# Performance work log

Hardware: AMD Instinct MI355X
Metric: run time of the kernel (lower is better)

The kernel has to match this reference:

```python
import jax, jax.numpy as jnp
import numpy as np

N_NODES = 100000
N_EDGES = 800000
NUM_GRAPHS = 512
IN_DIM = 16
EDGE_DIM = 1
HID = 64       # emb_dim
MLP_H = 32     # hidden_layers inside each MPNNLayer
L = 3          # num_layers
EPS = 1e-5


def setup_inputs() -> dict:
    key = jax.random.key(0)
    ks = jax.random.split(key, 24)
    s = 0.05
    inp = {
        "x": jax.random.normal(ks[0], (N_NODES, IN_DIM), jnp.float32),
        "edge_index": jax.random.randint(ks[1], (2, N_EDGES), 0, N_NODES),
        "edge_attr": jax.random.uniform(ks[2], (N_EDGES, EDGE_DIM), jnp.float32),
        "batch": jnp.sort(jax.random.randint(ks[3], (N_NODES,), 0, NUM_GRAPHS)),
        # input projection
        "lin_in_w": jax.random.normal(ks[4], (IN_DIM, HID), jnp.float32) * s,
        "lin_in_b": jnp.zeros((HID,), jnp.float32),
        # message MLP (stacked over L layers): Linear(129->32), BN(32), ReLU, Linear(32->64), ReLU, BN(64)
        "msg_w1": jax.random.normal(ks[5], (L, 2 * HID + EDGE_DIM, MLP_H), jnp.float32) * s,
        "msg_b1": jnp.zeros((L, MLP_H), jnp.float32),
        "msg_g1": jnp.ones((L, MLP_H), jnp.float32),
        "msg_be1": jnp.zeros((L, MLP_H), jnp.float32),
        "msg_w2": jax.random.normal(ks[6], (L, MLP_H, HID), jnp.float32) * s,
        "msg_b2": jnp.zeros((L, HID), jnp.float32),
        "msg_g2": jnp.ones((L, HID), jnp.float32),
        "msg_be2": jnp.zeros((L, HID), jnp.float32),
        # update MLP: Linear(128->32), BN(32), ReLU, Linear(32->64), ReLU, BN(64)
        "upd_w1": jax.random.normal(ks[7], (L, 2 * HID, MLP_H), jnp.float32) * s,
        "upd_b1": jnp.zeros((L, MLP_H), jnp.float32),
        "upd_g1": jnp.ones((L, MLP_H), jnp.float32),
        "upd_be1": jnp.zeros((L, MLP_H), jnp.float32),
        "upd_w2": jax.random.normal(ks[8], (L, MLP_H, HID), jnp.float32) * s,
        "upd_b2": jnp.zeros((L, HID), jnp.float32),
        "upd_g2": jnp.ones((L, HID), jnp.float32),
        "upd_be2": jnp.zeros((L, HID), jnp.float32),
        # head Linear(64->1) + ReLU
        "out_w": jax.random.normal(ks[9], (HID, 1), jnp.float32) * s,
        "out_b": jnp.zeros((1,), jnp.float32),
    }
    return inp


def _bn(h, g, b):
    # BatchNorm1d, training-mode batch stats (biased variance), dropout treated as identity (eval)
    mu = jnp.mean(h, axis=0)
    var = jnp.var(h, axis=0)
    return g * (h - mu) * jax.lax.rsqrt(var + EPS) + b


def reference(x, edge_index, edge_attr, batch,
              lin_in_w, lin_in_b,
              msg_w1, msg_b1, msg_g1, msg_be1, msg_w2, msg_b2, msg_g2, msg_be2,
              upd_w1, upd_b1, upd_g1, upd_be1, upd_w2, upd_b2, upd_g2, upd_be2,
              out_w, out_b):
    src = edge_index[0]  # x_j source
    dst = edge_index[1]  # x_i target / aggregation index
    h = x @ lin_in_w + lin_in_b  # [N, HID]
    for l in range(L):
        # message: cat([x_i, x_j, edge_attr]) -> Linear -> BN -> ReLU -> Linear -> ReLU -> BN
        m_in = jnp.concatenate([h[dst], h[src], edge_attr], axis=1)  # [E, 2*HID+EDGE_DIM]
        m = jax.nn.relu(_bn(m_in @ msg_w1[l] + msg_b1[l], msg_g1[l], msg_be1[l]))
        m = _bn(jax.nn.relu(m @ msg_w2[l] + msg_b2[l]), msg_g2[l], msg_be2[l])
        # aggregate: scatter-add over destination nodes
        agg = jax.ops.segment_sum(m, dst, num_segments=N_NODES)  # [N, HID]
        # update: cat([x, aggr]) -> Linear -> BN -> ReLU -> Linear -> ReLU -> BN
        u_in = jnp.concatenate([h, agg], axis=1)  # [N, 2*HID]
        u = jax.nn.relu(_bn(u_in @ upd_w1[l] + upd_b1[l], upd_g1[l], upd_be1[l]))
        u = _bn(jax.nn.relu(u @ upd_w2[l] + upd_b2[l]), upd_g2[l], upd_be2[l])
        h = h + u  # residual (x += conv(...))
    # global mean pool
    pooled = jax.ops.segment_sum(h, batch, num_segments=NUM_GRAPHS)
    counts = jax.ops.segment_sum(jnp.ones((h.shape[0],), h.dtype), batch, num_segments=NUM_GRAPHS)
    pooled = pooled / jnp.maximum(counts, 1.0)[:, None]
    return jax.nn.relu(pooled @ out_w + out_b).reshape(-1)  # [NUM_GRAPHS]
```

## Files before the change

### kernel.cpp

```cpp
#include <hip/hip_runtime.h>
#include <hip/hip_bf16.h>

#define N_NODES   100000
#define N_EDGES   800000
#define NUM_GRAPHS 512
#define IN_DIM    16
#define HID       64
#define MLP_H     32
#define EPS       1e-5f
#define TPB       256
#define SCAN_B    1024
#define NCHUNK    ((N_NODES + SCAN_B - 1) / SCAN_B)
#define GSB       2048
#define NWAVES    (GSB * 4)
#define PER_W     ((N_EDGES + NWAVES - 1) / NWAVES)
#define NODEBLKS  ((N_NODES + 63) / 64)

using nh2   = decltype(__builtin_amdgcn_cvt_pkrtz(0.f, 0.f));
typedef _Float16 f16x8 __attribute__((ext_vector_type(8)));
typedef float    f32x4 __attribute__((ext_vector_type(4)));
typedef int      i32x4 __attribute__((ext_vector_type(4)));

__device__ __forceinline__ nh2 pack2(float a, float b) {
  return __builtin_amdgcn_cvt_pkrtz(a, b);
}
__device__ __forceinline__ float wsum(float v) {
  v += __shfl_xor(v, 1, 64);
  v += __shfl_xor(v, 2, 64);
  v += __shfl_xor(v, 4, 64);
  v += __shfl_xor(v, 8, 64);
  v += __shfl_xor(v, 16, 64);
  v += __shfl_xor(v, 32, 64);
  return v;
}
__device__ __forceinline__ int lbound(const int* __restrict__ rs, int key) {
  int lo = 0, hi = N_NODES;
  while (lo < hi) { int m = (lo + hi) >> 1; if (rs[m] < key) lo = m + 1; else hi = m; }
  return lo;
}

__global__ __launch_bounds__(TPB) void k_deg(const int* __restrict__ ei, int* __restrict__ deg) {
  int e = blockIdx.x * TPB + threadIdx.x;
  if (e < N_EDGES) atomicAdd(&deg[ei[N_EDGES + e]], 1);
}

__global__ __launch_bounds__(SCAN_B) void k_scan_part(const int* __restrict__ deg,
                                                      int* __restrict__ partials) {
  __shared__ int red[SCAN_B];
  int i = blockIdx.x * SCAN_B + threadIdx.x;
  red[threadIdx.x] = (i < N_NODES) ? deg[i] : 0;
  __syncthreads();
  for (int off = SCAN_B / 2; off > 0; off >>= 1) {
    if (threadIdx.x < off) red[threadIdx.x] += red[threadIdx.x + off];
    __syncthreads();
  }
  if (threadIdx.x == 0) partials[blockIdx.x] = red[0];
}

__global__ void k_scan_mid(int* __restrict__ partials, int* __restrict__ row_start) {
  int run = 0;
  for (int b = 0; b < NCHUNK; ++b) { int t = partials[b]; partials[b] = run; run += t; }
  row_start[N_NODES] = run;
}

__global__ __launch_bounds__(SCAN_B) void k_scan_fin(const int* __restrict__ deg,
                                                     const int* __restrict__ partials,
                                                     int* __restrict__ row_start,
                                                     int* __restrict__ cursor) {
  __shared__ int buf[2][SCAN_B];
  int t = threadIdx.x, i = blockIdx.x * SCAN_B + t;
  int v = (i < N_NODES) ? deg[i] : 0;
  buf[0][t] = v;
  __syncthreads();
  int cur = 0;
  for (int off = 1; off < SCAN_B; off <<= 1) {
    int nv = buf[cur][t] + ((t >= off) ? buf[cur][t - off] : 0);
    buf[cur ^ 1][t] = nv; cur ^= 1;
    __syncthreads();
  }
  if (i < N_NODES) {
    int excl = buf[cur][t] - v + partials[blockIdx.x];
    row_start[i] = excl;
    cursor[i] = excl;
  }
}

__global__ __launch_bounds__(TPB) void k_fill(const int* __restrict__ ei,
                                              const float* __restrict__ ea,
                                              int* __restrict__ cursor,
                                              i32x4* __restrict__ erec) {
  int e = blockIdx.x * TPB + threadIdx.x;
  if (e >= N_EDGES) return;
  int dst = ei[N_EDGES + e];
  int pos = atomicAdd(&cursor[dst], 1);
  i32x4 rec;
  rec[0] = ei[e];
  rec[1] = dst;
  rec[2] = __float_as_int(ea[e]);
  rec[3] = 0;
  erec[pos] = rec;
}

__global__ __launch_bounds__(TPB) void k_lin_in(const float* __restrict__ x,
                                                const float* __restrict__ w,
                                                const float* __restrict__ b,
                                                float* __restrict__ h) {
  int i = blockIdx.x * TPB + threadIdx.x;
  if (i >= N_NODES) return;
  float xi[IN_DIM];
  const float4* xp = reinterpret_cast<const float4*>(x + i * IN_DIM);
#pragma unroll
  for (int q = 0; q < 4; ++q) {
    float4 v = xp[q];
    xi[4*q] = v.x; xi[4*q+1] = v.y; xi[4*q+2] = v.z; xi[4*q+3] = v.w;
  }
  float4* hp = reinterpret_cast<float4*>(h + i * HID);
#pragma unroll
  for (int j4 = 0; j4 < HID/4; ++j4) {
    float o[4];
#pragma unroll
    for (int c = 0; c < 4; ++c) {
      int j = j4*4 + c;
      float acc = b[j];
#pragma unroll
      for (int k = 0; k < IN_DIM; ++k) acc += xi[k] * w[k*HID + j];
      o[c] = acc;
    }
    float4 ov = {o[0], o[1], o[2], o[3]};
    hp[j4] = ov;
  }
}

__global__ __launch_bounds__(TPB) void k_pq(const float* __restrict__ h,
                                            const float* __restrict__ w1,
                                            const float* __restrict__ b1,
                                            _Float16* __restrict__ Ph,
                                            _Float16* __restrict__ Qh) {
  const int part = __builtin_amdgcn_readfirstlane(threadIdx.x >> 6);
  const int lane = threadIdx.x & 63;
  const int i = blockIdx.x * 64 + lane;
  if (i >= N_NODES) return;
  const int jb = (part & 1) * 16;
  const bool isQ = part >= 2;
  const float* wbase = w1 + (isQ ? 64 * MLP_H : 0) + jb;
  float acc[16];
#pragma unroll
  for (int j = 0; j < 16; ++j) acc[j] = isQ ? 0.f : b1[jb + j];
  const float4* hp = reinterpret_cast<const float4*>(h + i * HID);
#pragma unroll 4
  for (int k4 = 0; k4 < 16; ++k4) {
    float4 a = hp[k4];
    const float* wr = wbase + (k4*4) * MLP_H;
#pragma unroll
    for (int j = 0; j < 16; ++j)
      acc[j] += a.x*wr[j] + a.y*wr[MLP_H+j] + a.z*wr[2*MLP_H+j] + a.w*wr[3*MLP_H+j];
  }
  _Float16* dst = isQ ? Qh : Ph;
  i32x4 o0, o1;
#pragma unroll
  for (int c = 0; c < 4; ++c) {
    o0[c] = __builtin_bit_cast(int, pack2(acc[2*c],   acc[2*c+1]));
    o1[c] = __builtin_bit_cast(int, pack2(acc[8+2*c], acc[8+2*c+1]));
  }
  i32x4* qp = reinterpret_cast<i32x4*>(dst + i * MLP_H + jb);
  qp[0] = o0; qp[1] = o1;
}

__global__ __launch_bounds__(TPB) void k_gather(const _Float16* __restrict__ Ph,
                                                const _Float16* __restrict__ Qh,
                                                const i32x4* __restrict__ erec,
                                                const float* __restrict__ w1,
                                                _Float16* __restrict__ z1h,
                                                float* __restrict__ gstat) {
  const int lane = threadIdx.x & 63;
  const int kq  = lane & 15;
  const int qtr = lane >> 4;
  const float wk0 = w1[128 * MLP_H + 2*kq];
  const float wk1 = w1[128 * MLP_H + 2*kq + 1];
  const int* Qi = (const int*)Qh;
  const int* Pi = (const int*)Ph;
  int* z1i = (int*)z1h;
  float s0 = 0.f, s1 = 0.f, qa0 = 0.f, qa1 = 0.f;
  const int wv = blockIdx.x * 4 + (threadIdx.x >> 6);
  const int c0 = wv * PER_W;
  const int c1 = min(c0 + PER_W, N_EDGES);
  if (c0 < N_EDGES) {
    const int c1m1 = c1 - 1;
    const int rounds = (c1 - c0 + 3) >> 2;
#define EIDX(R) min(c0 + 4*(R) + qtr, c1m1)
    i32x4 rec2 = erec[EIDX(0)];
    i32x4 rec3 = erec[EIDX(1)];
    i32x4 recH = erec[EIDX(2)];
    int   qiA = Qi[rec2[0] * 16 + kq];
    int   piA = Pi[rec2[1] * 16 + kq];
    float aA  = __int_as_float(rec2[2]);
    int   qiB = Qi[rec3[0] * 16 + kq];
    int   piB = Pi[rec3[1] * 16 + kq];
    float aB  = __int_as_float(rec3[2]);
    for (int r = 0; r < rounds; ++r) {
      i32x4 recN = erec[EIDX(r + 3)];
      int   qiC = Qi[recH[0] * 16 + kq];
      int   piC = Pi[recH[1] * 16 + kq];
      float aC  = __int_as_float(recH[2]);
      const int e = c0 + 4*r + qtr;
      nh2 hv = __builtin_bit_cast(nh2, qiA);
      nh2 pv = __builtin_bit_cast(nh2, piA);
      float z0 = (float)pv.x + (float)hv.x + aA * wk0;
      float z1 = (float)pv.y + (float)hv.y + aA * wk1;
      if (e < c1) {
        z1i[min(e, c1m1) * 16 + kq] = __builtin_bit_cast(int, pack2(z0, z1));
        s0 += z0; s1 += z1;
        qa0 = fmaf(z0, z0, qa0); qa1 = fmaf(z1, z1, qa1);
      }
      qiA = qiB; piA = piB; aA = aB;
      qiB = qiC; piB = piC; aB = aC;
      recH = recN;
    }
#undef EIDX
  }
  s0  += __shfl_xor(s0, 16, 64);  s0  += __shfl_xor(s0, 32, 64);
  s1  += __shfl_xor(s1, 16, 64);  s1  += __shfl_xor(s1, 32, 64);
  qa0 += __shfl_xor(qa0, 16, 64); qa0 += __shfl_xor(qa0, 32, 64);
  qa1 += __shfl_xor(qa1, 16, 64); qa1 += __shfl_xor(qa1, 32, 64);
  __shared__ float ls[4][MLP_H], lq[4][MLP_H];
  const int w = threadIdx.x >> 6;
  if (lane < 16) {
    ls[w][2*lane] = s0; ls[w][2*lane+1] = s1;
    lq[w][2*lane] = qa0; lq[w][2*lane+1] = qa1;
  }
  __syncthreads();
  const int t = threadIdx.x;
  if (t < MLP_H)
    unsafeAtomicAdd(&gstat[t], ls[0][t] + ls[1][t] + ls[2][t] + ls[3][t]);
  else if (t < 2*MLP_H)
    unsafeAtomicAdd(&gstat[t], lq[0][t-MLP_H] + lq[1][t-MLP_H] + lq[2][t-MLP_H] + lq[3][t-MLP_H]);
}

__global__ __launch_bounds__(TPB) void k_msgdot(const _Float16* __restrict__ z1h,
                                                const int* __restrict__ rs,
                                                const float* __restrict__ gstat_in,
                                                const float* __restrict__ g1,
                                                const float* __restrict__ be1,
                                                const float* __restrict__ w2,
                                                const float* __restrict__ b2,
                                                float* __restrict__ agg,
                                                float* __restrict__ gstat_out) {
  const int lane = threadIdx.x & 63;
  const int col = lane & 15;
  const int g   = lane >> 4;
  float a1v[8], c1v[8];
#pragma unroll
  for (int i = 0; i < 8; ++i) {
    int kf = g*8 + i;
    float mu = gstat_in[kf] * (1.f / N_EDGES);
    float var = fmaxf(gstat_in[MLP_H + kf] * (1.f / N_EDGES) - mu * mu, 0.f);
    float a = g1[kf] * rsqrtf(var + EPS);
    a1v[i] = a; c1v[i] = be1[kf] - a * mu;
  }
  f16x8 bf0, bf1, bf2, bf3;
#define MKB(BF, C) { i32x4 bw; \
  _Pragma("unroll") for (int ii = 0; ii < 4; ++ii) { \
    nh2 p = pack2(w2[(g*8 + 2*ii) * HID + (C)*16 + col], \
                  w2[(g*8 + 2*ii + 1) * HID + (C)*16 + col]); \
    bw[ii] = __builtin_bit_cast(int, p); } \
  BF = __builtin_bit_cast(f16x8, bw); }
  MKB(bf0, 0) MKB(bf1, 1) MKB(bf2, 2) MKB(bf3, 3)
#undef MKB
  float b2c[4];
#pragma unroll
  for (int c = 0; c < 4; ++c) b2c[c] = b2[c*16 + col];

  float sacc[4] = {0.f,0.f,0.f,0.f}, qacc[4] = {0.f,0.f,0.f,0.f};
  const int wv = blockIdx.x * 4 + (threadIdx.x >> 6);
  const int key0 = min(wv * PER_W, N_EDGES);
  const int key1 = min((wv + 1) * PER_W, N_EDGES);
  const int n0 = lbound(rs, key0);
  const int n1 = (wv == NWAVES - 1) ? N_NODES : lbound(rs, key1);

  if (n0 < n1) {
    const int eLast = rs[n1] - 1;
    f16x8 zv = *reinterpret_cast<const f16x8*>(z1h + min(rs[n0] + col, eLast) * MLP_H + g * 8);
    for (int n = n0; n < n1; ++n) {
      const int start = rs[n], end = rs[n + 1];
      float aggacc[4] = {0.f,0.f,0.f,0.f};
      for (int t0 = start; t0 < end; t0 += 16) {
        const int bnext = (t0 + 16 < end) ? (t0 + 16) : end;
        f16x8 zvN = *reinterpret_cast<const f16x8*>(z1h + min(bnext + col, eLast) * MLP_H + g * 8);
        i32x4 aw;
#pragma unroll
        for (int i = 0; i < 4; ++i) {
          float m0 = fmaxf(fmaf(a1v[2*i],   (float)zv[2*i],   c1v[2*i]),   0.f);
          float m1 = fmaxf(fmaf(a1v[2*i+1], (float)zv[2*i+1], c1v[2*i+1]), 0.f);
          aw[i] = __builtin_bit_cast(int, pack2(m0, m1));
        }
        f16x8 af = __builtin_bit_cast(f16x8, aw);
        f32x4 zc = {0.f,0.f,0.f,0.f};
        f32x4 cc0 = __builtin_amdgcn_mfma_f32_16x16x32_f16(af, bf0, zc, 0, 0, 0);
        f32x4 cc1 = __builtin_amdgcn_mfma_f32_16x16x32_f16(af, bf1, zc, 0, 0, 0);
        f32x4 cc2 = __builtin_amdgcn_mfma_f32_16x16x32_f16(af, bf2, zc, 0, 0, 0);
        f32x4 cc3 = __builtin_amdgcn_mfma_f32_16x16x32_f16(af, bf3, zc, 0, 0, 0);
        bool vld[4];
#pragma unroll
        for (int reg = 0; reg < 4; ++reg) vld[reg] = (t0 + g*4 + reg) < end;
#define EPI(CC, CI) { \
  _Pragma("unroll") for (int reg = 0; reg < 4; ++reg) { \
    float tv = fmaxf(CC[reg] + b2c[CI], 0.f); \
    tv = vld[reg] ? tv : 0.f; \
    aggacc[CI] += tv; qacc[CI] = fmaf(tv, tv, qacc[CI]); } }
        EPI(cc0, 0) EPI(cc1, 1) EPI(cc2, 2) EPI(cc3, 3)
#undef EPI
        zv = zvN;
      }
#pragma unroll
      for (int c = 0; c < 4; ++c) sacc[c] += aggacc[c];
#pragma unroll
      for (int c = 0; c < 4; ++c) {
        aggacc[c] += __shfl_xor(aggacc[c], 16, 64);
        aggacc[c] += __shfl_xor(aggacc[c], 32, 64);
      }
      float aout = (g == 0) ? aggacc[0] : (g == 1) ? aggacc[1] : (g == 2) ? aggacc[2] : aggacc[3];
      agg[n * HID + g * 16 + col] = aout;
    }
  }
#pragma unroll
  for (int c = 0; c < 4; ++c) {
    sacc[c] += __shfl_xor(sacc[c], 16, 64);
    sacc[c] += __shfl_xor(sacc[c], 32, 64);
    qacc[c] += __shfl_xor(qacc[c], 16, 64);
    qacc[c] += __shfl_xor(qacc[c], 32, 64);
  }
  __shared__ float ls[4][HID], lq[4][HID];
  const int w = threadIdx.x >> 6;
  if (g == 0) {
#pragma unroll
    for (int c = 0; c < 4; ++c) { ls[w][c*16 + col] = sacc[c]; lq[w][c*16 + col] = qacc[c]; }
  }
  __syncthreads();
  const int t = threadIdx.x;
  if (t < HID)
    unsafeAtomicAdd(&gstat_out[t], ls[0][t] + ls[1][t] + ls[2][t] + ls[3][t]);
  else if (t < 2*HID)
    unsafeAtomicAdd(&gstat_out[t], lq[0][t-HID] + lq[1][t-HID] + lq[2][t-HID] + lq[3][t-HID]);
}

__global__ __launch_bounds__(TPB) void k_upd1(const float* __restrict__ h,
                                              const float* __restrict__ agg,
                                              const int* __restrict__ deg,
                                              const float* __restrict__ gstat_in,
                                              const float* __restrict__ g2,
                                              const float* __restrict__ be2,
                                              const float* __restrict__ w1,
                                              const float* __restrict__ b1,
                                              float* __restrict__ zu1) {
  __shared__ float sa[HID], sc[HID];
  {
    int t = threadIdx.x;
    if (t < HID) {
      float mu = gstat_in[t] * (1.f / N_EDGES);
      float var = fmaxf(gstat_in[HID + t] * (1.f / N_EDGES) - mu * mu, 0.f);
      float a = g2[t] * rsqrtf(var + EPS);
      sa[t] = a; sc[t] = be2[t] - a * mu;
    }
  }
  __syncthreads();
  const int widx = __builtin_amdgcn_readfirstlane(threadIdx.x >> 6);
  const int part = widx & 1;
  const int grp  = blockIdx.x * 2 + (widx >> 1);
  const int lane = threadIdx.x & 63;
  const int jb = part * 16;
  const int i = grp * 64 + lane;
  if (i >= N_NODES) return;
  float acc[16];
#pragma unroll
  for (int j = 0; j < 16; ++j) acc[j] = b1[jb + j];
  const float4* hp = reinterpret_cast<const float4*>(h + i * HID);
#pragma unroll 4
  for (int k4 = 0; k4 < 16; ++k4) {
    float4 a = hp[k4];
    const float* wr = w1 + (k4*4) * MLP_H + jb;
#pragma unroll
    for (int j = 0; j < 16; ++j)
      acc[j] += a.x*wr[j] + a.y*wr[MLP_H+j] + a.z*wr[2*MLP_H+j] + a.w*wr[3*MLP_H+j];
  }
  float degf = (float)deg[i];
  const float4* ap = reinterpret_cast<const float4*>(agg + i * HID);
#pragma unroll 4
  for (int k4 = 0; k4 < 16; ++k4) {
    float4 g4 = ap[k4];
    int k = k4*4;
    float a0 = sa[k]  *g4.x + sc[k]  *degf;
    float a1 = sa[k+1]*g4.y + sc[k+1]*degf;
    float a2 = sa[k+2]*g4.z + sc[k+2]*degf;
    float a3 = sa[k+3]*g4.w + sc[k+3]*degf;
    const float* wr = w1 + (64 + k) * MLP_H + jb;
#pragma unroll
    for (int j = 0; j < 16; ++j)
      acc[j] += a0*wr[j] + a1*wr[MLP_H+j] + a2*wr[2*MLP_H+j] + a3*wr[3*MLP_H+j];
  }
  float4* zp = reinterpret_cast<float4*>(zu1 + i * MLP_H + jb);
#pragma unroll
  for (int c = 0; c < 4; ++c) {
    float4 o = {acc[4*c], acc[4*c+1], acc[4*c+2], acc[4*c+3]};
    zp[c] = o;
  }
}

__global__ __launch_bounds__(TPB) void k_upd2(const float* __restrict__ zu1,
                                              const float* __restrict__ gstat_in,
                                              const float* __restrict__ gu1,
                                              const float* __restrict__ beu1,
                                              const float* __restrict__ w2,
                                              const float* __restrict__ b2,
                                              float* __restrict__ tu) {
  __shared__ float sa[MLP_H], sc[MLP_H];
  {
    int t = threadIdx.x;
    if (t < MLP_H) {
      float mu = gstat_in[t] * (1.f / N_NODES);
      float var = fmaxf(gstat_in[MLP_H + t] * (1.f / N_NODES) - mu * mu, 0.f);
      float a = gu1[t] * rsqrtf(var + EPS);
      sa[t] = a; sc[t] = beu1[t] - a * mu;
    }
  }
  __syncthreads();
  const int widx = __builtin_amdgcn_readfirstlane(threadIdx.x >> 6);
  const int part = widx & 1;
  const int grp  = blockIdx.x * 2 + (widx >> 1);
  const int lane = threadIdx.x & 63;
  const int jb = part * 32;
  const int i = grp * 64 + lane;
  if (i >= N_NODES) return;
  float m1[MLP_H];
  const float4* zp = reinterpret_cast<const float4*>(zu1 + i * MLP_H);
#pragma unroll
  for (int c = 0; c < MLP_H/4; ++c) {
    float4 z = zp[c];
    int kk = 4*c;
    m1[kk]   = fmaxf(sa[kk]  *z.x + sc[kk],   0.f);
    m1[kk+1] = fmaxf(sa[kk+1]*z.y + sc[kk+1], 0.f);
    m1[kk+2] = fmaxf(sa[kk+2]*z.z + sc[kk+2], 0.f);
    m1[kk+3] = fmaxf(sa[kk+3]*z.w + sc[kk+3], 0.f);
  }
#pragma unroll
  for (int j4 = 0; j4 < 8; ++j4) {
    float tv[4];
#pragma unroll
    for (int c = 0; c < 4; ++c) {
      int j = jb + j4*4 + c;
      float v = b2[j];
#pragma unroll
      for (int kk = 0; kk < MLP_H; ++kk) v += m1[kk] * w2[kk*HID + j];
      tv[c] = fmaxf(v, 0.f);
    }
    float4 o = {tv[0], tv[1], tv[2], tv[3]};
    *reinterpret_cast<float4*>(tu + i * HID + jb + j4*4) = o;
  }
}

template <int NF>
__global__ __launch_bounds__(TPB) void k_colstats(const float* __restrict__ X,
                                                  int nrows, float* __restrict__ gstat) {
  const int RPB = TPB / NF;
  int f = threadIdx.x % NF;
  int rloc = threadIdx.x / NF;
  float s = 0.f, q = 0.f;
  for (int r = blockIdx.x * RPB + rloc; r < nrows; r += gridDim.x * RPB) {
    float v = X[r * NF + f];
    s += v; q = fmaf(v, v, q);
  }
  __shared__ float ls[TPB], lq[TPB];
  ls[threadIdx.x] = s; lq[threadIdx.x] = q;
  __syncthreads();
  if (threadIdx.x < NF) {
    float ss = 0.f, qq = 0.f;
#pragma unroll
    for (int r = 0; r < RPB; ++r) { ss += ls[r*NF + f]; qq += lq[r*NF + f]; }
    unsafeAtomicAdd(&gstat[f], ss);
    unsafeAtomicAdd(&gstat[NF + f], qq);
  }
}

__global__ __launch_bounds__(TPB) void k_resid(float* __restrict__ h,
                                               const float* __restrict__ tu,
                                               const float* __restrict__ gstat_in,
                                               const float* __restrict__ gu2,
                                               const float* __restrict__ beu2) {
  __shared__ float sa[HID], sc[HID];
  {
    int t = threadIdx.x;
    if (t < HID) {
      float mu = gstat_in[t] * (1.f / N_NODES);
      float var = fmaxf(gstat_in[HID + t] * (1.f / N_NODES) - mu * mu, 0.f);
      float a = gu2[t] * rsqrtf(var + EPS);
      sa[t] = a; sc[t] = beu2[t] - a * mu;
    }
  }
  __syncthreads();
  int idx = blockIdx.x * TPB + threadIdx.x;
  if (idx >= N_NODES * (HID/4)) return;
  int j0 = (idx & (HID/4 - 1)) * 4;
  float4 hv = reinterpret_cast<const float4*>(h)[idx];
  float4 tv = reinterpret_cast<const float4*>(tu)[idx];
  hv.x += sa[j0]  *tv.x + sc[j0];
  hv.y += sa[j0+1]*tv.y + sc[j0+1];
  hv.z += sa[j0+2]*tv.z + sc[j0+2];
  hv.w += sa[j0+3]*tv.w + sc[j0+3];
  reinterpret_cast<float4*>(h)[idx] = hv;
}

__global__ __launch_bounds__(TPB) void k_pool_head(const float* __restrict__ h,
                                                   const int* __restrict__ batch,
                                                   const float* __restrict__ ow,
                                                   const float* __restrict__ ob,
                                                   float* __restrict__ out) {
  int g = blockIdx.x;
  int lo = 0, hi = N_NODES;
  while (lo < hi) { int mid = (lo+hi) >> 1; if (batch[mid] < g) lo = mid+1; else hi = mid; }
  int start = lo;
  lo = start; hi = N_NODES;
  while (lo < hi) { int mid = (lo+hi) >> 1; if (batch[mid] < g+1) lo = mid+1; else hi = mid; }
  int end = lo;
  int j = threadIdx.x & 63;
  int sub = threadIdx.x >> 6;
  float acc = 0.f;
  for (int n = start + sub; n < end; n += 4) acc += h[n*HID + j];
  __shared__ float red[TPB];
  red[threadIdx.x] = acc;
  __syncthreads();
  if (threadIdx.x < 64) {
    float s = red[threadIdx.x] + red[64+threadIdx.x] + red[128+threadIdx.x] + red[192+threadIdx.x];
    float cnt = (float)(end - start);
    float pooled = s / fmaxf(cnt, 1.0f);
    float v = pooled * ow[threadIdx.x];
    v = wsum(v);
    if (threadIdx.x == 0) out[g] = fmaxf(v + ob[0], 0.f);
  }
}

extern "C" void kernel_launch(void* const* d_in, const int* in_sizes, int n_in,
                              void* d_out, int out_size, void* d_ws, size_t ws_size,
                              hipStream_t stream) {
  const float* x       = (const float*)d_in[0];
  const int*   ei      = (const int*)  d_in[1];
  const float* ea      = (const float*)d_in[2];
  const int*   batch   = (const int*)  d_in[3];
  const float* lin_w   = (const float*)d_in[4];
  const float* lin_b   = (const float*)d_in[5];
  const float* msg_w1  = (const float*)d_in[6];
  const float* msg_b1  = (const float*)d_in[7];
  const float* msg_g1  = (const float*)d_in[8];
  const float* msg_be1 = (const float*)d_in[9];
  const float* msg_w2  = (const float*)d_in[10];
  const float* msg_b2  = (const float*)d_in[11];
  const float* msg_g2  = (const float*)d_in[12];
  const float* msg_be2 = (const float*)d_in[13];
  const float* upd_w1  = (const float*)d_in[14];
  const float* upd_b1  = (const float*)d_in[15];
  const float* upd_g1  = (const float*)d_in[16];
  const float* upd_be1 = (const float*)d_in[17];
  const float* upd_w2  = (const float*)d_in[18];
  const float* upd_b2  = (const float*)d_in[19];
  const float* upd_g2  = (const float*)d_in[20];
  const float* upd_be2 = (const float*)d_in[21];
  const float* out_w   = (const float*)d_in[22];
  const float* out_b   = (const float*)d_in[23];
  float* out = (float*)d_out;

  float* W     = (float*)d_ws;
  float* h     = W;
  _Float16* Ph = (_Float16*)(W + 6400000);
  _Float16* Qh = (_Float16*)(W + 9600000);
  float* agg   = W + 12800000;
  _Float16* z1h = (_Float16*)(W + 19200000);
  float* zu1   = W + 32000000;
  float* tu    = W + 35200000;
  float* stats = W + 41600000;
  int*   ib    = (int*)(W + 41601152);
  int* deg       = ib;
  int* row_start = ib + 100000;
  int* cursor    = ib + 200001;
  int* partials  = ib + 300001;
  i32x4* erec    = (i32x4*)(ib + 300232);

  hipMemsetAsync(stats, 0, 3*384*sizeof(float), stream);
  hipMemsetAsync(deg, 0, N_NODES*sizeof(int), stream);

  k_deg<<<N_EDGES/TPB, TPB, 0, stream>>>(ei, deg);
  k_scan_part<<<NCHUNK, SCAN_B, 0, stream>>>(deg, partials);
  k_scan_mid<<<1, 1, 0, stream>>>(partials, row_start);
  k_scan_fin<<<NCHUNK, SCAN_B, 0, stream>>>(deg, partials, row_start, cursor);
  k_fill<<<N_EDGES/TPB, TPB, 0, stream>>>(ei, ea, cursor, erec);

  k_lin_in<<<(N_NODES+TPB-1)/TPB, TPB, 0, stream>>>(x, lin_w, lin_b, h);

  const int PQ_BLKS  = NODEBLKS;
  const int UPD_BLKS = (NODEBLKS + 1) / 2;

  for (int l = 0; l < 3; ++l) {
    const float* mw1 = msg_w1 + (size_t)l*129*MLP_H;
    const float* mb1 = msg_b1 + l*MLP_H;
    const float* mg1 = msg_g1 + l*MLP_H;
    const float* mbe1= msg_be1 + l*MLP_H;
    const float* mw2 = msg_w2 + (size_t)l*MLP_H*HID;
    const float* mb2 = msg_b2 + l*HID;
    const float* mg2 = msg_g2 + l*HID;
    const float* mbe2= msg_be2 + l*HID;
    const float* uw1 = upd_w1 + (size_t)l*128*MLP_H;
    const float* ub1 = upd_b1 + l*MLP_H;
    const float* ug1 = upd_g1 + l*MLP_H;
    const float* ube1= upd_be1 + l*MLP_H;
    const float* uw2 = upd_w2 + (size_t)l*MLP_H*HID;
    const float* ub2 = upd_b2 + l*HID;
    const float* ug2 = upd_g2 + l*HID;
    const float* ube2= upd_be2 + l*HID;
    float* st = stats + l*384;

    k_pq<<<PQ_BLKS, TPB, 0, stream>>>(h, mw1, mb1, Ph, Qh);
    k_gather<<<GSB, TPB, 0, stream>>>(Ph, Qh, erec, mw1, z1h, st);
    k_msgdot<<<GSB, TPB, 0, stream>>>(z1h, row_start, st, mg1, mbe1, mw2, mb2, agg, st+64);
    k_upd1<<<UPD_BLKS, TPB, 0, stream>>>(h, agg, deg, st+64, mg2, mbe2, uw1, ub1, zu1);
    k_colstats<MLP_H><<<512, TPB, 0, stream>>>(zu1, N_NODES, st+192);
    k_upd2<<<UPD_BLKS, TPB, 0, stream>>>(zu1, st+192, ug1, ube1, uw2, ub2, tu);
    k_colstats<HID><<<512, TPB, 0, stream>>>(tu, N_NODES, st+256);
    k_resid<<<(N_NODES*(HID/4)+TPB-1)/TPB, TPB, 0, stream>>>(h, tu, st+256, ug2, ube2);
  }

  k_pool_head<<<NUM_GRAPHS, TPB, 0, stream>>>(h, batch, out_w, out_b, out);
}
```

Baseline: 944.8 us.

## Balance msgdot work with precomputed 16-edge tile map instead of node ranges

Builds a tile map in preprocessing, splitting each destination node's edge list into 16-edge tiles, and gives each wave an equal count of tiles instead of binary-searching node ranges by edge count. Nodes whose tiles span wave boundaries are combined with atomic adds, so agg is zeroed with a memset every layer. This removes per-wave binary searches and wasted MFMA lanes from partial node tiles, and evens out load across waves. In exchange it adds a second scan, a tile-map kernel, a per-layer memset of agg and some atomics.

```diff
diff --git a/kernel.cpp b/kernel.cpp
--- a/kernel.cpp
+++ b/kernel.cpp
@@ -15,6 +15,7 @@
 #define NWAVES    (GSB * 4)
 #define PER_W     ((N_EDGES + NWAVES - 1) / NWAVES)
 #define NODEBLKS  ((N_NODES + 63) / 64)
+#define NTILE_MAX 150016
 
 using nh2   = decltype(__builtin_amdgcn_cvt_pkrtz(0.f, 0.f));
 typedef _Float16 f16x8 __attribute__((ext_vector_type(8)));
@@ -33,22 +34,19 @@
   v += __shfl_xor(v, 32, 64);
   return v;
 }
-__device__ __forceinline__ int lbound(const int* __restrict__ rs, int key) {
-  int lo = 0, hi = N_NODES;
-  while (lo < hi) { int m = (lo + hi) >> 1; if (rs[m] < key) lo = m + 1; else hi = m; }
-  return lo;
-}
 
 __global__ __launch_bounds__(TPB) void k_deg(const int* __restrict__ ei, int* __restrict__ deg) {
   int e = blockIdx.x * TPB + threadIdx.x;
   if (e < N_EDGES) atomicAdd(&deg[ei[N_EDGES + e]], 1);
 }
 
+template <int MODE>
 __global__ __launch_bounds__(SCAN_B) void k_scan_part(const int* __restrict__ deg,
                                                       int* __restrict__ partials) {
   __shared__ int red[SCAN_B];
   int i = blockIdx.x * SCAN_B + threadIdx.x;
-  red[threadIdx.x] = (i < N_NODES) ? deg[i] : 0;
+  int v = (i < N_NODES) ? deg[i] : 0;
+  red[threadIdx.x] = MODE ? ((v + 15) >> 4) : v;
   __syncthreads();
   for (int off = SCAN_B / 2; off > 0; off >>= 1) {
     if (threadIdx.x < off) red[threadIdx.x] += red[threadIdx.x + off];
@@ -57,19 +55,21 @@
   if (threadIdx.x == 0) partials[blockIdx.x] = red[0];
 }
 
-__global__ void k_scan_mid(int* __restrict__ partials, int* __restrict__ row_start) {
+__global__ void k_scan_mid(int* __restrict__ partials, int* __restrict__ total_out) {
   int run = 0;
   for (int b = 0; b < NCHUNK; ++b) { int t = partials[b]; partials[b] = run; run += t; }
-  row_start[N_NODES] = run;
-}
-
+  total_out[N_NODES] = run;
+}
+
+template <int MODE>
 __global__ __launch_bounds__(SCAN_B) void k_scan_fin(const int* __restrict__ deg,
                                                      const int* __restrict__ partials,
-                                                     int* __restrict__ row_start,
+                                                     int* __restrict__ out_start,
                                                      int* __restrict__ cursor) {
   __shared__ int buf[2][SCAN_B];
   int t = threadIdx.x, i = blockIdx.x * SCAN_B + t;
-  int v = (i < N_NODES) ? deg[i] : 0;
+  int raw = (i < N_NODES) ? deg[i] : 0;
+  int v = MODE ? ((raw + 15) >> 4) : raw;
   buf[0][t] = v;
   __syncthreads();
   int cur = 0;
@@ -80,8 +80,8 @@
   }
   if (i < N_NODES) {
     int excl = buf[cur][t] - v + partials[blockIdx.x];
-    row_start[i] = excl;
-    cursor[i] = excl;
+    out_start[i] = excl;
+    if (cursor) cursor[i] = excl;
   }
 }
 
@@ -99,6 +99,26 @@
   rec[2] = __float_as_int(ea[e]);
   rec[3] = 0;
   erec[pos] = rec;
+}
+
+__global__ __launch_bounds__(TPB) void k_tmap(const int* __restrict__ deg,
+                                              const int* __restrict__ row_start,
+                                              const int* __restrict__ tile_start,
+                                              int* __restrict__ tmap,
+                                              int* __restrict__ te0) {
+  int n = blockIdx.x * TPB + threadIdx.x;
+  if (n >= N_NODES) return;
+  int d = deg[n];
+  if (d == 0) return;
+  int ts = tile_start[n];
+  int es = row_start[n];
+  int gcnt = (d + 15) >> 4;
+  for (int j = 0; j < gcnt; ++j) {
+    int vcnt = d - 16 * j; if (vcnt > 16) vcnt = 16;
+    int flags = (j == 0 ? (1 << 30) : 0) | (j == gcnt - 1 ? (1 << 31) : 0);
+    tmap[ts + j] = n | (vcnt << 20) | flags;
+    te0[ts + j] = es + 16 * j;
+  }
 }
 
 __global__ __launch_bounds__(TPB) void k_lin_in(const float* __restrict__ x,
@@ -237,7 +257,9 @@
 }
 
 __global__ __launch_bounds__(TPB) void k_msgdot(const _Float16* __restrict__ z1h,
-                                                const int* __restrict__ rs,
+                                                const int* __restrict__ tmap,
+                                                const int* __restrict__ te0,
+                                                const int* __restrict__ tile_total,
                                                 const float* __restrict__ gstat_in,
                                                 const float* __restrict__ g1,
                                                 const float* __restrict__ be1,
@@ -271,55 +293,82 @@
   for (int c = 0; c < 4; ++c) b2c[c] = b2[c*16 + col];
 
   float sacc[4] = {0.f,0.f,0.f,0.f}, qacc[4] = {0.f,0.f,0.f,0.f};
+  const int ntiles = tile_total[N_NODES];
+  const int tpw = (ntiles + NWAVES - 1) / NWAVES;
   const int wv = blockIdx.x * 4 + (threadIdx.x >> 6);
-  const int key0 = min(wv * PER_W, N_EDGES);
-  const int key1 = min((wv + 1) * PER_W, N_EDGES);
-  const int n0 = lbound(rs, key0);
-  const int n1 = (wv == NWAVES - 1) ? N_NODES : lbound(rs, key1);
-
-  if (n0 < n1) {
-    const int eLast = rs[n1] - 1;
-    f16x8 zv = *reinterpret_cast<const f16x8*>(z1h + min(rs[n0] + col, eLast) * MLP_H + g * 8);
-    for (int n = n0; n < n1; ++n) {
-      const int start = rs[n], end = rs[n + 1];
-      float aggacc[4] = {0.f,0.f,0.f,0.f};
-      for (int t0 = start; t0 < end; t0 += 16) {
-        const int bnext = (t0 + 16 < end) ? (t0 + 16) : end;
-        f16x8 zvN = *reinterpret_cast<const f16x8*>(z1h + min(bnext + col, eLast) * MLP_H + g * 8);
-        i32x4 aw;
-#pragma unroll
-        for (int i = 0; i < 4; ++i) {
-          float m0 = fmaxf(fmaf(a1v[2*i],   (float)zv[2*i],   c1v[2*i]),   0.f);
-          float m1 = fmaxf(fmaf(a1v[2*i+1], (float)zv[2*i+1], c1v[2*i+1]), 0.f);
-          aw[i] = __builtin_bit_cast(int, pack2(m0, m1));
-        }
-        f16x8 af = __builtin_bit_cast(f16x8, aw);
-        f32x4 zc = {0.f,0.f,0.f,0.f};
-        f32x4 cc0 = __builtin_amdgcn_mfma_f32_16x16x32_f16(af, bf0, zc, 0, 0, 0);
-        f32x4 cc1 = __builtin_amdgcn_mfma_f32_16x16x32_f16(af, bf1, zc, 0, 0, 0);
-        f32x4 cc2 = __builtin_amdgcn_mfma_f32_16x16x32_f16(af, bf2, zc, 0, 0, 0);
-        f32x4 cc3 = __builtin_amdgcn_mfma_f32_16x16x32_f16(af, bf3, zc, 0, 0, 0);
-        bool vld[4];
-#pragma unroll
-        for (int reg = 0; reg < 4; ++reg) vld[reg] = (t0 + g*4 + reg) < end;
+  const int tb = wv * tpw;
+  const int te = min(tb + tpw, ntiles);
+  const int eLast = N_EDGES - 1;
+
+  if (tb < te) {
+    int tm = __builtin_amdgcn_readfirstlane(tmap[tb]);
+    int t0 = __builtin_amdgcn_readfirstlane(te0[tb]);
+    f16x8 zv = *reinterpret_cast<const f16x8*>(z1h + min(t0 + col, eLast) * MLP_H + g * 8);
+    int cur = -1;
+    bool sawFirst = false;
+    float aggacc[4] = {0.f,0.f,0.f,0.f};
+    for (int t = tb; t < te; ++t) {
+      const int tn = min(t + 1, ntiles - 1);
+      const int tmN = __builtin_amdgcn_readfirstlane(tmap[tn]);
+      const int t0N = __builtin_amdgcn_readfirstlane(te0[tn]);
+      f16x8 zvN = *reinterpret_cast<const f16x8*>(z1h + min(t0N + col, eLast) * MLP_H + g * 8);
+      const int node = tm & 0xFFFFF;
+      const int vcnt = (tm >> 20) & 31;
+      const bool first = (tm >> 30) & 1;
+      const bool last  = (tm >> 31) & 1;
+      if (cur < 0) { cur = node; sawFirst = first; }
+      i32x4 aw;
+#pragma unroll
+      for (int i = 0; i < 4; ++i) {
+        float m0 = fmaxf(fmaf(a1v[2*i],   (float)zv[2*i],   c1v[2*i]),   0.f);
+        float m1 = fmaxf(fmaf(a1v[2*i+1], (float)zv[2*i+1], c1v[2*i+1]), 0.f);
+        aw[i] = __builtin_bit_cast(int, pack2(m0, m1));
+      }
+      f16x8 af = __builtin_bit_cast(f16x8, aw);
+      f32x4 zc = {0.f,0.f,0.f,0.f};
+      f32x4 cc0 = __builtin_amdgcn_mfma_f32_16x16x32_f16(af, bf0, zc, 0, 0, 0);
+      f32x4 cc1 = __builtin_amdgcn_mfma_f32_16x16x32_f16(af, bf1, zc, 0, 0, 0);
+      f32x4 cc2 = __builtin_amdgcn_mfma_f32_16x16x32_f16(af, bf2, zc, 0, 0, 0);
+      f32x4 cc3 = __builtin_amdgcn_mfma_f32_16x16x32_f16(af, bf3, zc, 0, 0, 0);
+      bool vld[4];
+#pragma unroll
+      for (int reg = 0; reg < 4; ++reg) vld[reg] = (g*4 + reg) < vcnt;
 #define EPI(CC, CI) { \
   _Pragma("unroll") for (int reg = 0; reg < 4; ++reg) { \
     float tv = fmaxf(CC[reg] + b2c[CI], 0.f); \
     tv = vld[reg] ? tv : 0.f; \
-    aggacc[CI] += tv; qacc[CI] = fmaf(tv, tv, qacc[CI]); } }
-        EPI(cc0, 0) EPI(cc1, 1) EPI(cc2, 2) EPI(cc3, 3)
+    aggacc[CI] += tv; sacc[CI] += tv; qacc[CI] = fmaf(tv, tv, qacc[CI]); } }
+      EPI(cc0, 0) EPI(cc1, 1) EPI(cc2, 2) EPI(cc3, 3)
 #undef EPI
-        zv = zvN;
+      if (last) {
+        float rr[4];
+#pragma unroll
+        for (int c = 0; c < 4; ++c) {
+          float v = aggacc[c];
+          v += __shfl_xor(v, 16, 64);
+          v += __shfl_xor(v, 32, 64);
+          rr[c] = v;
+        }
+        float aout = (g == 0) ? rr[0] : (g == 1) ? rr[1] : (g == 2) ? rr[2] : rr[3];
+        if (sawFirst) agg[cur * HID + g * 16 + col] = aout;
+        else          unsafeAtomicAdd(&agg[cur * HID + g * 16 + col], aout);
+        cur = -1;
+#pragma unroll
+        for (int c = 0; c < 4; ++c) aggacc[c] = 0.f;
       }
-#pragma unroll
-      for (int c = 0; c < 4; ++c) sacc[c] += aggacc[c];
+      tm = tmN; t0 = t0N; zv = zvN;
+    }
+    if (cur >= 0) {
+      float rr[4];
 #pragma unroll
       for (int c = 0; c < 4; ++c) {
-        aggacc[c] += __shfl_xor(aggacc[c], 16, 64);
-        aggacc[c] += __shfl_xor(aggacc[c], 32, 64);
+        float v = aggacc[c];
+        v += __shfl_xor(v, 16, 64);
+        v += __shfl_xor(v, 32, 64);
+        rr[c] = v;
       }
-      float aout = (g == 0) ? aggacc[0] : (g == 1) ? aggacc[1] : (g == 2) ? aggacc[2] : aggacc[3];
-      agg[n * HID + g * 16 + col] = aout;
+      float aout = (g == 0) ? rr[0] : (g == 1) ? rr[1] : (g == 2) ? rr[2] : rr[3];
+      unsafeAtomicAdd(&agg[cur * HID + g * 16 + col], aout);
     }
   }
 #pragma unroll
@@ -576,20 +625,28 @@
   float* tu    = W + 35200000;
   float* stats = W + 41600000;
   int*   ib    = (int*)(W + 41601152);
-  int* deg       = ib;
-  int* row_start = ib + 100000;
-  int* cursor    = ib + 200001;
-  int* partials  = ib + 300001;
-  i32x4* erec    = (i32x4*)(ib + 300232);
+  int* deg        = ib;
+  int* row_start  = ib + 100000;
+  int* cursor     = ib + 200001;
+  int* partials   = ib + 300001;
+  int* tile_start = ib + 300136;
+  int* partials2  = ib + 400137;
+  int* tmap       = ib + 400272;
+  int* te0        = ib + 550288;
+  i32x4* erec     = (i32x4*)(ib + 700308);
 
   hipMemsetAsync(stats, 0, 3*384*sizeof(float), stream);
   hipMemsetAsync(deg, 0, N_NODES*sizeof(int), stream);
 
   k_deg<<<N_EDGES/TPB, TPB, 0, stream>>>(ei, deg);
-  k_scan_part<<<NCHUNK, SCAN_B, 0, stream>>>(deg, partials);
+  k_scan_part<0><<<NCHUNK, SCAN_B, 0, stream>>>(deg, partials);
   k_scan_mid<<<1, 1, 0, stream>>>(partials, row_start);
-  k_scan_fin<<<NCHUNK, SCAN_B, 0, stream>>>(deg, partials, row_start, cursor);
+  k_scan_fin<0><<<NCHUNK, SCAN_B, 0, stream>>>(deg, partials, row_start, cursor);
+  k_scan_part<1><<<NCHUNK, SCAN_B, 0, stream>>>(deg, partials2);
+  k_scan_mid<<<1, 1, 0, stream>>>(partials2, tile_start);
+  k_scan_fin<1><<<NCHUNK, SCAN_B, 0, stream>>>(deg, partials2, tile_start, (int*)nullptr);
   k_fill<<<N_EDGES/TPB, TPB, 0, stream>>>(ei, ea, cursor, erec);
+  k_tmap<<<(N_NODES+TPB-1)/TPB, TPB, 0, stream>>>(deg, row_start, tile_start, tmap, te0);
 
   k_lin_in<<<(N_NODES+TPB-1)/TPB, TPB, 0, stream>>>(x, lin_w, lin_b, h);
 
@@ -615,9 +672,11 @@
     const float* ube2= upd_be2 + l*HID;
     float* st = stats + l*384;
 
+    hipMemsetAsync(agg, 0, (size_t)N_NODES*HID*sizeof(float), stream);
     k_pq<<<PQ_BLKS, TPB, 0, stream>>>(h, mw1, mb1, Ph, Qh);
     k_gather<<<GSB, TPB, 0, stream>>>(Ph, Qh, erec, mw1, z1h, st);
-    k_msgdot<<<GSB, TPB, 0, stream>>>(z1h, row_start, st, mg1, mbe1, mw2, mb2, agg, st+64);
+    k_msgdot<<<GSB, TPB, 0, stream>>>(z1h, tmap, te0, tile_start, st, mg1, mbe1, mw2, mb2,
+                                      agg, st+64);
     k_upd1<<<UPD_BLKS, TPB, 0, stream>>>(h, agg, deg, st+64, mg2, mbe2, uw1, ub1, zu1);
     k_colstats<MLP_H><<<512, TPB, 0, stream>>>(zu1, N_NODES, st+192);
     k_upd2<<<UPD_BLKS, TPB, 0, stream>>>(zu1, st+192, ug1, ube1, uw2, ub2, tu);
```

Result: no change. 952.6 us (+0.8%).
